# Optimization experiments

Measured on AMD Instinct MI355X. Metric: run time of the kernel, lower is better.

Reference implementation:

```python
import jax, jax.numpy as jnp
import numpy as np

# Constructor constants (init_kwargs)
DX = 10.0        # grid spacing [m]
DT = 0.001       # time step [s]
PML_FREQ = 15.0  # dominant frequency (used only for PML design in deepwave; see notes)
PML = 35         # pml_width
HALF = 4         # half-width of 8th-order stencil
NY, NX = 100, 200
NT = 300
N_SHOTS, N_SRC, N_REC = 2, 1, 100

# 8th-order central second-derivative coefficients, offsets -4..4
C2 = np.array([-1/560, 8/315, -1/5, 8/5, -205/72, 8/5, -1/5, 8/315, -1/560], np.float32)
# 8th-order central first-derivative coefficients, offsets -4..4
C1 = np.array([1/280, -4/105, 1/5, -4/5, 0.0, 4/5, -1/5, 4/105, -1/280], np.float32)


def shift_sum(u, coefs, axis):
    """Apply a 9-tap 1D stencil along `axis` (zero boundary outside the padded grid)."""
    pad = [(0, 0)] * u.ndim
    pad[axis] = (HALF, HALF)
    up = jnp.pad(u, pad)
    n = u.shape[axis]
    acc = jnp.zeros_like(u)
    for k in range(2 * HALF + 1):
        sl = [slice(None)] * u.ndim
        sl[axis] = slice(k, k + n)
        acc = acc + coefs[k] * up[tuple(sl)]
    return acc


def _sigma(n, vmax):
    # Quadratic PML damping profile, sigma_max from R=1e-3 reflection coefficient.
    d = jnp.arange(n, dtype=jnp.float32)
    r = jnp.maximum(jnp.maximum((PML - d) / PML, (d - (n - 1 - PML)) / PML), 0.0)
    smax = 3.0 * vmax * np.float32(np.log(1000.0)) / (2.0 * PML * DX)
    return smax * r * r


def _propagate(vp, src, src_loc, rec_loc):
    S, _, nt = src.shape
    v = jnp.pad(vp, PML, mode="edge")          # [ny, nx] padded grid
    ny, nx = v.shape
    v2 = (v * v)[None]                           # [1, ny, nx]
    vmax = jnp.max(vp)
    sy = _sigma(ny, vmax)
    sx = _sigma(nx, vmax)
    s = (sy[:, None] + sx[None, :])[None]        # combined damping
    pr = (sy[:, None] * sx[None, :])[None]       # corner cross term
    by = jnp.exp(-sy * DT)[None, :, None]        # CPML recursion factors
    bx = jnp.exp(-sx * DT)[None, None, :]
    c2 = jnp.asarray(C2) / np.float32(DX * DX)
    c1 = jnp.asarray(C1) / np.float32(DX)
    sids = jnp.arange(S)[:, None]
    syi = src_loc[..., 0] + PML
    sxi = src_loc[..., 1] + PML
    ryi = rec_loc[..., 0] + PML
    rxi = rec_loc[..., 1] + PML
    dt2 = np.float32(DT * DT)

    def step(carry, f_t):
        u, um, py, px = carry
        # CPML memory variables for the first derivatives
        py = by * py + (by - 1.0) * shift_sum(u, c1, 1)
        px = bx * px + (bx - 1.0) * shift_sum(u, c1, 2)
        lap = (shift_sum(u, c2, 1) + shift_sum(u, c2, 2)
               + shift_sum(py, c1, 1) + shift_sum(px, c1, 2))
        f = jnp.zeros_like(u).at[sids, syi, sxi].add(f_t)
        un = ((2.0 - pr * dt2) * u - (1.0 - 0.5 * s * DT) * um
              + dt2 * v2 * (lap + f)) / (1.0 + 0.5 * s * DT)
        rec = un[sids, ryi, rxi]                 # [S, n_rec]
        return (un, u, py, px), rec

    z = jnp.zeros((S, ny, nx), vp.dtype)
    xs = jnp.moveaxis(src, -1, 0)                # [nt, S, n_src]
    _, recs = jax.lax.scan(jax.checkpoint(step), (z, z, z, z), xs)
    return jnp.moveaxis(recs, 0, -1)             # [S, n_rec, nt]


def setup_inputs() -> dict:
    key = jax.random.key(0)
    k1, k2, k3, k4 = jax.random.split(key, 4)
    vp = 1500.0 + 2500.0 * jax.random.uniform(k1, (NY, NX), jnp.float32)
    src = jax.random.normal(k2, (N_SHOTS, N_SRC, NT), jnp.float32)
    src_loc = jax.random.randint(k3, (N_SHOTS, N_SRC, 2), 0, 90)
    rec_loc = jax.random.randint(k4, (N_SHOTS, N_REC, 2), 0, 90)
    return {"vp": vp, "src": src, "src_loc": src_loc, "rec_loc": rec_loc}


def reference(vp, src, src_loc, rec_loc):
    vx = _propagate(vp, src, src_loc, rec_loc)   # [S, n_rec, nt]
    # wrapper: vx.permute(0, 2, 1).unsqueeze(0) -> [1, S, nt, n_rec]
    return jnp.transpose(vx, (0, 2, 1))[None]
```

## Files before the change

### kernel.cpp

```cpp
#include <hip/hip_runtime.h>

constexpr int NY = 100, NX = 200;
constexpr int PML = 35;
constexpr int NYP = 170, NXP = 270;
constexpr int S = 2, NREC = 100, NT = 300;
constexpr float DX = 10.0f, DT = 1e-3f, DT2 = DT * DT;

constexpr int NTY = 16, NTX = 8;
constexpr int TY = 11, TX = 34;
constexpr int NBLKS = S * NTY * NTX;
constexpr int THREADS = 768;

constexpr int UTS = 35;
constexpr int UTSZ = TX * UTS;
constexpr int URS = 51;
constexpr int URSZ = TY * URS;
constexpr int PTS = 19;
constexpr int PTSZ = TX * PTS;
constexpr int PXS = 43;
constexpr int PXSZ = TY * PXS;
constexpr int BYW = TY + 8;
constexpr int BXW = TX + 8;

constexpr int CELLS_NS = 8 * TX;
constexpr int CELLS_WE = TY * 8;
constexpr int OFF_N = 0;
constexpr int OFF_S = CELLS_NS;
constexpr int OFF_W = 2 * CELLS_NS;
constexpr int OFF_E = 2 * CELLS_NS + CELLS_WE;
constexpr int STAGE_CELLS = 2 * CELLS_NS + 2 * CELLS_WE;

typedef unsigned long long u64;

__device__ __constant__ float C2D[9] = {
    (float)(-1.0/560.0/100.0), (float)(8.0/315.0/100.0), (float)(-1.0/5.0/100.0),
    (float)(8.0/5.0/100.0),    (float)(-205.0/72.0/100.0), (float)(8.0/5.0/100.0),
    (float)(-1.0/5.0/100.0),   (float)(8.0/315.0/100.0),  (float)(-1.0/560.0/100.0)};
__device__ __constant__ float C1D[9] = {
    (float)(1.0/280.0/10.0), (float)(-4.0/105.0/10.0), (float)(1.0/5.0/10.0),
    (float)(-4.0/5.0/10.0),  0.0f,                     (float)(4.0/5.0/10.0),
    (float)(-1.0/5.0/10.0),  (float)(4.0/105.0/10.0),  (float)(-1.0/280.0/10.0)};

__device__ __forceinline__ u64 gload64(const u64* p) {
    return __hip_atomic_load(p, __ATOMIC_RELAXED, __HIP_MEMORY_SCOPE_AGENT);
}
__device__ __forceinline__ void gstore64(u64* p, u64 v) {
    __hip_atomic_store(p, v, __ATOMIC_RELAXED, __HIP_MEMORY_SCOPE_AGENT);
}

__device__ __forceinline__ float sigma_of(int d, int n, float smax) {
    float r = fmaxf(fmaxf((float)(PML - d) / (float)PML,
                          (float)(d - (n - 1 - PML)) / (float)PML), 0.0f);
    return smax * r * r;
}

__global__ void vmax_kernel(const float* __restrict__ vp, float* __restrict__ cst) {
    __shared__ float red[256];
    float m = 0.0f;
    for (int i = threadIdx.x; i < NY * NX; i += 256) m = fmaxf(m, vp[i]);
    red[threadIdx.x] = m;
    __syncthreads();
    for (int s2 = 128; s2 > 0; s2 >>= 1) {
        if (threadIdx.x < s2) red[threadIdx.x] = fmaxf(red[threadIdx.x], red[threadIdx.x + s2]);
        __syncthreads();
    }
    if (threadIdx.x == 0)
        cst[0] = 3.0f * red[0] * logf(1000.0f) / (2.0f * PML * DX);
}

__global__ __launch_bounds__(THREADS) void persist_kernel(
    const float* __restrict__ vp, const float* __restrict__ src,
    const int* __restrict__ src_loc, const int* __restrict__ rec_loc,
    float* __restrict__ out, u64* __restrict__ stage,
    const float* __restrict__ cst) {

    __shared__ float uT[2][UTSZ];
    __shared__ float uR[2][URSZ];
    __shared__ float pyT[2][PTSZ];
    __shared__ float pxR[2][PXSZ];
    __shared__ float byS[BYW], bymS[BYW], bxS[BXW], bxmS[BXW];
    __shared__ float srcS[NT];

    const int tid = threadIdx.x;
    const int bid = blockIdx.x;
    const int sh  = bid / (NTY * NTX);
    const int tr  = bid - sh * (NTY * NTX);
    const int tyi = tr / NTX, txi = tr - tyi * NTX;
    const int y0 = tyi * TY, x0 = txi * TX;
    const int rows = min(TY, NYP - y0), cols = min(TX, NXP - x0);
    const float smax = cst[0];

    for (int i = tid; i < 2 * UTSZ; i += THREADS) ((float*)uT)[i] = 0.0f;
    for (int i = tid; i < 2 * URSZ; i += THREADS) ((float*)uR)[i] = 0.0f;
    for (int i = tid; i < 2 * PTSZ; i += THREADS) ((float*)pyT)[i] = 0.0f;
    for (int i = tid; i < 2 * PXSZ; i += THREADS) ((float*)pxR)[i] = 0.0f;

    if (tid < BYW) {
        int yy = y0 - 4 + tid;
        if (yy >= 0 && yy < NYP) {
            float b = __expf(-sigma_of(yy, NYP, smax) * DT);
            byS[tid] = b; bymS[tid] = b - 1.0f;
        } else { byS[tid] = 0.0f; bymS[tid] = 0.0f; }
    }
    if (tid < BXW) {
        int xx = x0 - 4 + tid;
        if (xx >= 0 && xx < NXP) {
            float b = __expf(-sigma_of(xx, NXP, smax) * DT);
            bxS[tid] = b; bxmS[tid] = b - 1.0f;
        } else { bxS[tid] = 0.0f; bxmS[tid] = 0.0f; }
    }

    const int role = tid & 1;
    const int cell = tid >> 1;
    const bool hasTask = (tid < 2 * rows * cols);
    const int y = hasTask ? cell / cols : 0;
    const int x = hasTask ? cell - y * cols : 0;

    float e_r = 0.0f, d_r = 0.0f, Av_r = 0.0f, Bv_r = 0.0f;
    if (hasTask) {
        int gy = y0 + y, gx = x0 + x;
        int vy = min(max(gy - PML, 0), NY - 1), vx = min(max(gx - PML, 0), NX - 1);
        float v = vp[vy * NX + vx];
        e_r = DT2 * v * v;
        float syv = sigma_of(gy, NYP, smax), sxv = sigma_of(gx, NXP, smax);
        d_r  = 1.0f / (1.0f + 0.5f * (syv + sxv) * DT);
        Av_r = 2.0f - syv * sxv * DT2;
        Bv_r = 1.0f - 0.5f * (syv + sxv) * DT;
    }

    const int sy = src_loc[sh * 2 + 0] + PML, sx = src_loc[sh * 2 + 1] + PML;
    const bool ownSrc = (sy >= y0 && sy < y0 + rows && sx >= x0 && sx < x0 + cols);
    const bool isSrc = hasTask && ownSrc && (y == sy - y0) && (x == sx - x0);
    if (ownSrc)
        for (int i = tid; i < NT; i += THREADS) srcS[i] = src[sh * NT + i];

    int recLds = -1, recOut = 0;
    if (tid < S * NREC) {
        int rs = tid / NREC, rr2 = tid - rs * NREC;
        int ry = rec_loc[(rs * NREC + rr2) * 2 + 0] + PML;
        int rx = rec_loc[(rs * NREC + rr2) * 2 + 1] + PML;
        if (rs == sh && ry >= y0 && ry < y0 + rows && rx >= x0 && rx < x0 + cols) {
            recLds = (ry - y0) * URS + (rx - x0 + 8);
            recOut = rs * NT * NREC + rr2;
        }
    }

    const int bN = (tyi > 0)       ? bid - NTX : -1;
    const int bS = (tyi < NTY - 1) ? bid + NTX : -1;
    const int bW = (txi > 0)       ? bid - 1   : -1;
    const int bE = (txi < NTX - 1) ? bid + 1   : -1;

    const int nNS = 8 * cols, nWE = rows * 8;
    const int nTot = 2 * nNS + 2 * nWE;

    int hOff = -1, hSrc = 0, hTgt = 0;
    if (tid < nTot) {
        int j = tid, nb = -1, o = 0, off = -1, tgt = 0;
        if (j < nNS) {
            nb = bN;
            int r2 = j / cols, c2 = j - r2 * cols;
            o = OFF_S + r2 * TX + c2;
            off = c2 * UTS + r2; tgt = 0;
        } else if ((j -= nNS) < nNS) {
            nb = bS;
            int r2 = j / cols, c2 = j - r2 * cols;
            if (nb >= 0) {
                int rowsS = min(TY, NYP - (y0 + TY));
                if (r2 >= rowsS) nb = -1;
            }
            o = OFF_N + r2 * TX + c2;
            off = c2 * UTS + (8 + rows + r2); tgt = 0;
        } else if ((j -= nNS) < nWE) {
            nb = bW;
            o = OFF_E + j;
            off = (j >> 3) * URS + (j & 7); tgt = 1;
        } else {
            j -= nWE;
            nb = bE;
            o = OFF_W + j;
            off = (j >> 3) * URS + 8 + cols + (j & 7); tgt = 1;
        }
        if (nb >= 0) { hOff = off; hTgt = tgt; hSrc = nb * 2 * STAGE_CELLS + o; }
    }
    const bool nv = (hOff >= 0);
    const u64* sA = stage + hSrc;

    int aN = -1, aS = -1, aW = -1, aE = -1;
    if (hasTask && role == 0) {
        if (y < 8)          aN = OFF_N + y * TX + x;
        if (y >= rows - 8)  aS = OFF_S + (y - (rows - 8)) * TX + x;
        if (x < 8)          aW = OFF_W + y * 8 + x;
        if (x >= cols - 8)  aE = OFF_E + y * 8 + (x - (cols - 8));
    }

    {
        const u64 PK0 = ((u64)1 << 32);
        u64* s0 = stage + (size_t)(bid * 2 + 0) * STAGE_CELLS;
        if (aN >= 0) gstore64(s0 + aN, PK0);
        if (aS >= 0) gstore64(s0 + aS, PK0);
        if (aW >= 0) gstore64(s0 + aW, PK0);
        if (aE >= 0) gstore64(s0 + aE, PK0);
    }
    __syncthreads();

    float wU[17], cbp[9];
    float bb0 = 0, bbm0 = 0, bb4 = 0, bbm4 = 0, bb8 = 0, bbm8 = 0;
    {
        float tb[9], tbm[9];
#pragma unroll
        for (int j = 0; j < 9; j++) {
            tb[j]  = hasTask ? (role ? bxS[x + j]  : byS[y + j])  : 0.0f;
            tbm[j] = hasTask ? (role ? bxmS[x + j] : bymS[y + j]) : 0.0f;
        }
#pragma unroll
        for (int n = 0; n < 17; n++) {
            float w = (n >= 4 && n <= 12) ? C2D[n - 4] : 0.0f;
#pragma unroll
            for (int k = 0; k < 9; k++) {
                int m = n - k;
                if (m >= 0 && m < 9)
                    w = fmaf(C1D[k] * tbm[k], C1D[m], w);
            }
            wU[n] = w;
        }
#pragma unroll
        for (int k = 0; k < 9; k++) cbp[k] = C1D[k] * tb[k];
        bb0 = tb[0]; bbm0 = tbm[0];
        bb4 = tb[4]; bbm4 = tbm[4];
        bb8 = tb[8]; bbm8 = tbm[8];
    }

    u64 pf = nv ? gload64(sA) : 0;

    float u_curr = 0.0f, u_prev = 0.0f;

    int pa = 0;
    for (int t = 0; t < NT; t++) {
        const int par = t & 1;
        float* uTc = uT[pa];       float* uRc = uR[pa];
        float* uTn = uT[pa ^ 1];   float* uRn = uR[pa ^ 1];
        const float* pyO = pyT[pa]; float* pyN = pyT[pa ^ 1];
        const float* pxO = pxR[pa]; float* pxN = pxR[pa ^ 1];

        if (nv) {
            const int need = t + 1;
            const u64* sp = sA + (size_t)par * STAGE_CELLS;
            while ((int)(pf >> 32) < need) pf = gload64(sp);
            (hTgt ? uRc : uTc)[hOff] = __uint_as_float((unsigned)pf);
        }
        __syncthreads();

        u64* sb = stage + (size_t)(bid * 2 + (par ^ 1)) * STAGE_CELLS;
        float up[17], pO[9], u_new = 0.0f;
        if (hasTask) {
            const float* uSrc = role ? &uRc[y * URS + x] : &uTc[x * UTS + y];
            const float* pSrc = role ? &pxO[y * PXS + x] : &pyO[x * PTS + y];

#pragma unroll
            for (int j = 0; j < 17; j++)
                up[j] = (j == 8) ? u_curr : uSrc[j];
#pragma unroll
            for (int k = 0; k < 9; k++) pO[k] = pSrc[k];

            float a0 = 0.0f, a1 = 0.0f, a2 = 0.0f, a3 = 0.0f;
#pragma unroll
            for (int n = 0; n < 16; n += 4) {
                a0 = fmaf(wU[n],     up[n],     a0);
                a1 = fmaf(wU[n + 1], up[n + 1], a1);
                a2 = fmaf(wU[n + 2], up[n + 2], a2);
                a3 = fmaf(wU[n + 3], up[n + 3], a3);
            }
            a0 = fmaf(wU[16], up[16], a0);
#pragma unroll
            for (int k = 0; k < 8; k += 4) {
                a0 = fmaf(cbp[k],     pO[k],     a0);
                a1 = fmaf(cbp[k + 1], pO[k + 1], a1);
                a2 = fmaf(cbp[k + 2], pO[k + 2], a2);
                a3 = fmaf(cbp[k + 3], pO[k + 3], a3);
            }
            a1 = fmaf(cbp[8], pO[8], a1);
            const float partial = (a0 + a1) + (a2 + a3);
            const float other = __shfl_xor(partial, 1);

            const float lap = partial + other;
            const float f = isSrc ? srcS[t] : 0.0f;
            u_new = (Av_r * u_curr - Bv_r * u_prev + e_r * (lap + f)) * d_r;

            const u64 pk = ((u64)(unsigned)(t + 2) << 32) |
                           (u64)__float_as_uint(u_new);
            if (aN >= 0) gstore64(sb + aN, pk);
            if (aS >= 0) gstore64(sb + aS, pk);
            if (aW >= 0) gstore64(sb + aW, pk);
            if (aE >= 0) gstore64(sb + aE, pk);
        }

        if (nv) pf = gload64(sA + (size_t)(par ^ 1) * STAGE_CELLS);

        if (hasTask) {
            float* pDst = role ? &pxR[pa ^ 1][y * PXS + x] : &pyT[pa ^ 1][x * PTS + y];
            float* uDst = role ? &uRn[y * URS + x + 8] : &uTn[x * UTS + y + 8];
            uDst[0] = u_new;
            {
                float d1u4 = 0.0f;
#pragma unroll
                for (int m = 0; m < 9; m++) d1u4 = fmaf(C1D[m], up[4 + m], d1u4);
                pDst[4] = fmaf(bb4, pO[4], bbm4 * d1u4);
            }
            const int lo = role ? x : y;
            const int hiLim = role ? cols : rows;
            if (lo < 4) {
                float d1u0 = 0.0f;
#pragma unroll
                for (int m = 0; m < 9; m++) d1u0 = fmaf(C1D[m], up[m], d1u0);
                pDst[0] = fmaf(bb0, pO[0], bbm0 * d1u0);
            }
            if (lo >= hiLim - 4) {
                float d1u8 = 0.0f;
#pragma unroll
                for (int m = 0; m < 9; m++) d1u8 = fmaf(C1D[m], up[8 + m], d1u8);
                pDst[8] = fmaf(bb8, pO[8], bbm8 * d1u8);
            }
            u_prev = u_curr; u_curr = u_new;
        }

        if (t > 0 && recLds >= 0) out[recOut + (t - 1) * NREC] = uRc[recLds];

        pa ^= 1;
    }

    __syncthreads();
    if (recLds >= 0) out[recOut + (NT - 1) * NREC] = uR[pa][recLds];
}

extern "C" void kernel_launch(void* const* d_in, const int* in_sizes, int n_in,
                              void* d_out, int out_size, void* d_ws, size_t ws_size,
                              hipStream_t stream) {
    const float* vp = (const float*)d_in[0];
    const float* src = (const float*)d_in[1];
    const int* src_loc = (const int*)d_in[2];
    const int* rec_loc = (const int*)d_in[3];
    float* out = (float*)d_out;

    float* ws = (float*)d_ws;
    float* cst = ws;
    u64* stage = (u64*)(ws + 32);

    hipMemsetAsync(d_ws, 0,
                   (size_t)32 * sizeof(float) +
                   (size_t)NBLKS * 2 * STAGE_CELLS * sizeof(u64),
                   stream);
    vmax_kernel<<<1, 256, 0, stream>>>(vp, cst);
    persist_kernel<<<NBLKS, THREADS, 0, stream>>>(
        vp, src, src_loc, rec_loc, out, stage, cst);
}
```

Before: 637.9 us.

## Register-block two cells per lane in 2x2 quads with shuffle-combined Laplacian

Each thread now computes a 1D stencil pass for two adjacent cells, so four lanes cover a 2x2 quad and exchange partial sums via shuffles. Loaded u and p windows are reused across both outputs, which cuts LDS reads per cell. The tile changes to 12x34 with 15 row blocks and 512 threads, and halo staging is spread over two entries per thread. It raises register pressure and makes every lane write both transposed u copies, and the quad mapping assumes even tile dimensions.

```diff
diff --git a/kernel.cpp b/kernel.cpp
--- a/kernel.cpp
+++ b/kernel.cpp
@@ -6,16 +6,16 @@
 constexpr int S = 2, NREC = 100, NT = 300;
 constexpr float DX = 10.0f, DT = 1e-3f, DT2 = DT * DT;
 
-constexpr int NTY = 16, NTX = 8;
-constexpr int TY = 11, TX = 34;
+constexpr int NTY = 15, NTX = 8;
+constexpr int TY = 12, TX = 34;
 constexpr int NBLKS = S * NTY * NTX;
-constexpr int THREADS = 768;
-
-constexpr int UTS = 35;
+constexpr int THREADS = 512;
+
+constexpr int UTS = 29;
 constexpr int UTSZ = TX * UTS;
 constexpr int URS = 51;
 constexpr int URSZ = TY * URS;
-constexpr int PTS = 19;
+constexpr int PTS = 21;
 constexpr int PTSZ = TX * PTS;
 constexpr int PXS = 43;
 constexpr int PXSZ = TY * PXS;
@@ -29,6 +29,7 @@
 constexpr int OFF_W = 2 * CELLS_NS;
 constexpr int OFF_E = 2 * CELLS_NS + CELLS_WE;
 constexpr int STAGE_CELLS = 2 * CELLS_NS + 2 * CELLS_WE;
+constexpr int NE = 2;
 
 typedef unsigned long long u64;
 
@@ -110,15 +111,20 @@
         } else { bxS[tid] = 0.0f; bxmS[tid] = 0.0f; }
     }
 
-    const int role = tid & 1;
-    const int cell = tid >> 1;
-    const bool hasTask = (tid < 2 * rows * cols);
-    const int y = hasTask ? cell / cols : 0;
-    const int x = hasTask ? cell - y * cols : 0;
+    const int l   = tid & 3;
+    const int qid = tid >> 2;
+    const int nQX = cols >> 1;
+    const int nQuads = (rows >> 1) * nQX;
+    const bool hasQ = (qid < nQuads);
+    const int qy = hasQ ? qid / nQX : 0;
+    const int qx = hasQ ? qid - qy * nQX : 0;
+    const bool isCol = (l < 2);
+    const int yp = 2 * qy + ((l == 1 || l == 3) ? 1 : 0);
+    const int xp = 2 * qx + ((l == 1 || l == 2) ? 1 : 0);
 
     float e_r = 0.0f, d_r = 0.0f, Av_r = 0.0f, Bv_r = 0.0f;
-    if (hasTask) {
-        int gy = y0 + y, gx = x0 + x;
+    if (hasQ) {
+        int gy = y0 + yp, gx = x0 + xp;
         int vy = min(max(gy - PML, 0), NY - 1), vx = min(max(gx - PML, 0), NX - 1);
         float v = vp[vy * NX + vx];
         e_r = DT2 * v * v;
@@ -130,7 +136,7 @@
 
     const int sy = src_loc[sh * 2 + 0] + PML, sx = src_loc[sh * 2 + 1] + PML;
     const bool ownSrc = (sy >= y0 && sy < y0 + rows && sx >= x0 && sx < x0 + cols);
-    const bool isSrc = hasTask && ownSrc && (y == sy - y0) && (x == sx - x0);
+    const bool isSrc = hasQ && ownSrc && (yp == sy - y0) && (xp == sx - x0);
     if (ownSrc)
         for (int i = tid; i < NT; i += THREADS) srcS[i] = src[sh * NT + i];
 
@@ -153,9 +159,14 @@
     const int nNS = 8 * cols, nWE = rows * 8;
     const int nTot = 2 * nNS + 2 * nWE;
 
-    int hOff = -1, hSrc = 0, hTgt = 0;
-    if (tid < nTot) {
-        int j = tid, nb = -1, o = 0, off = -1, tgt = 0;
+    int hOff[NE], hSrcI[NE], hTgt[NE];
+#pragma unroll
+    for (int e = 0; e < NE; e++) { hOff[e] = -1; hSrcI[e] = 0; hTgt[e] = 0; }
+#pragma unroll
+    for (int e = 0; e < NE; e++) {
+        int i = tid + e * THREADS;
+        if (i >= nTot) continue;
+        int j = i, nb = -1, o = 0, off = -1, tgt = 0;
         if (j < nNS) {
             nb = bN;
             int r2 = j / cols, c2 = j - r2 * cols;
@@ -180,17 +191,19 @@
             o = OFF_W + j;
             off = (j >> 3) * URS + 8 + cols + (j & 7); tgt = 1;
         }
-        if (nb >= 0) { hOff = off; hTgt = tgt; hSrc = nb * 2 * STAGE_CELLS + o; }
-    }
-    const bool nv = (hOff >= 0);
-    const u64* sA = stage + hSrc;
+        if (nb >= 0) { hOff[e] = off; hTgt[e] = tgt; hSrcI[e] = nb * 2 * STAGE_CELLS + o; }
+    }
+    bool nv[NE];
+    const u64* sA[NE];
+#pragma unroll
+    for (int e = 0; e < NE; e++) { nv[e] = (hOff[e] >= 0); sA[e] = stage + hSrcI[e]; }
 
     int aN = -1, aS = -1, aW = -1, aE = -1;
-    if (hasTask && role == 0) {
-        if (y < 8)          aN = OFF_N + y * TX + x;
-        if (y >= rows - 8)  aS = OFF_S + (y - (rows - 8)) * TX + x;
-        if (x < 8)          aW = OFF_W + y * 8 + x;
-        if (x >= cols - 8)  aE = OFF_E + y * 8 + (x - (cols - 8));
+    if (hasQ) {
+        if (yp < 8)          aN = OFF_N + yp * TX + xp;
+        if (yp >= rows - 8)  aS = OFF_S + (yp - (rows - 8)) * TX + xp;
+        if (xp < 8)          aW = OFF_W + yp * 8 + xp;
+        if (xp >= cols - 8)  aE = OFF_E + yp * 8 + (xp - (cols - 8));
     }
 
     {
@@ -203,34 +216,38 @@
     }
     __syncthreads();
 
-    float wU[17], cbp[9];
-    float bb0 = 0, bbm0 = 0, bb4 = 0, bbm4 = 0, bb8 = 0, bbm8 = 0;
-    {
-        float tb[9], tbm[9];
-#pragma unroll
-        for (int j = 0; j < 9; j++) {
-            tb[j]  = hasTask ? (role ? bxS[x + j]  : byS[y + j])  : 0.0f;
-            tbm[j] = hasTask ? (role ? bxmS[x + j] : bymS[y + j]) : 0.0f;
-        }
-#pragma unroll
-        for (int n = 0; n < 17; n++) {
-            float w = (n >= 4 && n <= 12) ? C2D[n - 4] : 0.0f;
-#pragma unroll
-            for (int k = 0; k < 9; k++) {
-                int m = n - k;
-                if (m >= 0 && m < 9)
-                    w = fmaf(C1D[k] * tbm[k], C1D[m], w);
-            }
-            wU[n] = w;
-        }
-#pragma unroll
-        for (int k = 0; k < 9; k++) cbp[k] = C1D[k] * tb[k];
-        bb0 = tb[0]; bbm0 = tbm[0];
-        bb4 = tb[4]; bbm4 = tbm[4];
-        bb8 = tb[8]; bbm8 = tbm[8];
-    }
-
-    u64 pf = nv ? gload64(sA) : 0;
+    const int base = isCol ? 2 * qy : 2 * qx;
+    const int lim  = isCol ? rows : cols;
+    float tb[10], tbm[10];
+#pragma unroll
+    for (int j = 0; j < 10; j++) {
+        tb[j]  = hasQ ? (isCol ? byS[base + j]  : bxS[base + j])  : 0.0f;
+        tbm[j] = hasQ ? (isCol ? bymS[base + j] : bxmS[base + j]) : 0.0f;
+    }
+    float wU0[17], wU1[17], cbp0[9], cbp1[9];
+#pragma unroll
+    for (int n = 0; n < 17; n++) {
+        float w0 = (n >= 4 && n <= 12) ? C2D[n - 4] : 0.0f;
+        float w1 = w0;
+#pragma unroll
+        for (int k = 0; k < 9; k++) {
+            int m = n - k;
+            if (m >= 0 && m < 9) {
+                w0 = fmaf(C1D[k] * tbm[k],     C1D[m], w0);
+                w1 = fmaf(C1D[k] * tbm[k + 1], C1D[m], w1);
+            }
+        }
+        wU0[n] = w0; wU1[n] = w1;
+    }
+#pragma unroll
+    for (int k = 0; k < 9; k++) {
+        cbp0[k] = C1D[k] * tb[k];
+        cbp1[k] = C1D[k] * tb[k + 1];
+    }
+
+    u64 pf[NE];
+#pragma unroll
+    for (int e = 0; e < NE; e++) pf[e] = nv[e] ? gload64(sA[e]) : 0;
 
     float u_curr = 0.0f, u_prev = 0.0f;
 
@@ -242,50 +259,79 @@
         const float* pyO = pyT[pa]; float* pyN = pyT[pa ^ 1];
         const float* pxO = pxR[pa]; float* pxN = pxR[pa ^ 1];
 
-        if (nv) {
+        {
             const int need = t + 1;
-            const u64* sp = sA + (size_t)par * STAGE_CELLS;
-            while ((int)(pf >> 32) < need) pf = gload64(sp);
-            (hTgt ? uRc : uTc)[hOff] = __uint_as_float((unsigned)pf);
+            for (;;) {
+                bool ok = true;
+#pragma unroll
+                for (int e = 0; e < NE; e++)
+                    if (nv[e] && (int)(pf[e] >> 32) < need) {
+                        pf[e] = gload64(sA[e] + (size_t)par * STAGE_CELLS);
+                        ok = false;
+                    }
+                if (ok) break;
+            }
+#pragma unroll
+            for (int e = 0; e < NE; e++)
+                if (nv[e]) (hTgt[e] ? uRc : uTc)[hOff[e]] = __uint_as_float((unsigned)pf[e]);
         }
         __syncthreads();
 
+        float uw[18], pw[10];
+        float p0 = 0.0f, p1 = 0.0f;
+        if (hasQ) {
+            const float* uW = isCol ? &uTc[(2 * qx + (l & 1)) * UTS + 2 * qy]
+                                    : &uRc[(2 * qy + (l & 1)) * URS + 2 * qx];
+            const float* pW = isCol ? &pyO[(2 * qx + (l & 1)) * PTS + 2 * qy]
+                                    : &pxO[(2 * qy + (l & 1)) * PXS + 2 * qx];
+#pragma unroll
+            for (int j = 0; j < 18; j++) uw[j] = uW[j];
+#pragma unroll
+            for (int k = 0; k < 10; k++) pw[k] = pW[k];
+
+            float a0 = 0, a1 = 0, a2 = 0, a3 = 0, b0 = 0, b1 = 0, b2 = 0, b3 = 0;
+#pragma unroll
+            for (int n = 0; n < 16; n += 4) {
+                a0 = fmaf(wU0[n],     uw[n],     a0);
+                a1 = fmaf(wU0[n + 1], uw[n + 1], a1);
+                a2 = fmaf(wU0[n + 2], uw[n + 2], a2);
+                a3 = fmaf(wU0[n + 3], uw[n + 3], a3);
+                b0 = fmaf(wU1[n],     uw[n + 1], b0);
+                b1 = fmaf(wU1[n + 1], uw[n + 2], b1);
+                b2 = fmaf(wU1[n + 2], uw[n + 3], b2);
+                b3 = fmaf(wU1[n + 3], uw[n + 4], b3);
+            }
+            a0 = fmaf(wU0[16], uw[16], a0);
+            b0 = fmaf(wU1[16], uw[17], b0);
+#pragma unroll
+            for (int k = 0; k < 8; k += 4) {
+                a0 = fmaf(cbp0[k],     pw[k],     a0);
+                a1 = fmaf(cbp0[k + 1], pw[k + 1], a1);
+                a2 = fmaf(cbp0[k + 2], pw[k + 2], a2);
+                a3 = fmaf(cbp0[k + 3], pw[k + 3], a3);
+                b0 = fmaf(cbp1[k],     pw[k + 1], b0);
+                b1 = fmaf(cbp1[k + 1], pw[k + 2], b1);
+                b2 = fmaf(cbp1[k + 2], pw[k + 3], b2);
+                b3 = fmaf(cbp1[k + 3], pw[k + 4], b3);
+            }
+            a1 = fmaf(cbp0[8], pw[8], a1);
+            b1 = fmaf(cbp1[8], pw[9], b1);
+            p0 = (a0 + a1) + (a2 + a3);
+            p1 = (b0 + b1) + (b2 + b3);
+        }
+
+        const float sh1 = __shfl_xor(p0, 2);
+        const float sh2 = __shfl_xor(p1, 2);
+        const float sh3 = __shfl_xor((l & 1) ? p0 : p1, 3);
+
         u64* sb = stage + (size_t)(bid * 2 + (par ^ 1)) * STAGE_CELLS;
-        float up[17], pO[9], u_new = 0.0f;
-        if (hasTask) {
-            const float* uSrc = role ? &uRc[y * URS + x] : &uTc[x * UTS + y];
-            const float* pSrc = role ? &pxO[y * PXS + x] : &pyO[x * PTS + y];
-
-#pragma unroll
-            for (int j = 0; j < 17; j++)
-                up[j] = (j == 8) ? u_curr : uSrc[j];
-#pragma unroll
-            for (int k = 0; k < 9; k++) pO[k] = pSrc[k];
-
-            float a0 = 0.0f, a1 = 0.0f, a2 = 0.0f, a3 = 0.0f;
-#pragma unroll
-            for (int n = 0; n < 16; n += 4) {
-                a0 = fmaf(wU[n],     up[n],     a0);
-                a1 = fmaf(wU[n + 1], up[n + 1], a1);
-                a2 = fmaf(wU[n + 2], up[n + 2], a2);
-                a3 = fmaf(wU[n + 3], up[n + 3], a3);
-            }
-            a0 = fmaf(wU[16], up[16], a0);
-#pragma unroll
-            for (int k = 0; k < 8; k += 4) {
-                a0 = fmaf(cbp[k],     pO[k],     a0);
-                a1 = fmaf(cbp[k + 1], pO[k + 1], a1);
-                a2 = fmaf(cbp[k + 2], pO[k + 2], a2);
-                a3 = fmaf(cbp[k + 3], pO[k + 3], a3);
-            }
-            a1 = fmaf(cbp[8], pO[8], a1);
-            const float partial = (a0 + a1) + (a2 + a3);
-            const float other = __shfl_xor(partial, 1);
-
-            const float lap = partial + other;
+        float u_new = 0.0f;
+        if (hasQ) {
+            const float lap = (l == 0) ? p0 + sh1 :
+                              (l == 1) ? p1 + sh2 :
+                              (l == 2) ? p1 + sh3 : p0 + sh3;
             const float f = isSrc ? srcS[t] : 0.0f;
             u_new = (Av_r * u_curr - Bv_r * u_prev + e_r * (lap + f)) * d_r;
-
             const u64 pk = ((u64)(unsigned)(t + 2) << 32) |
                            (u64)__float_as_uint(u_new);
             if (aN >= 0) gstore64(sb + aN, pk);
@@ -294,31 +340,43 @@
             if (aE >= 0) gstore64(sb + aE, pk);
         }
 
-        if (nv) pf = gload64(sA + (size_t)(par ^ 1) * STAGE_CELLS);
-
-        if (hasTask) {
-            float* pDst = role ? &pxR[pa ^ 1][y * PXS + x] : &pyT[pa ^ 1][x * PTS + y];
-            float* uDst = role ? &uRn[y * URS + x + 8] : &uTn[x * UTS + y + 8];
-            uDst[0] = u_new;
-            {
-                float d1u4 = 0.0f;
-#pragma unroll
-                for (int m = 0; m < 9; m++) d1u4 = fmaf(C1D[m], up[4 + m], d1u4);
-                pDst[4] = fmaf(bb4, pO[4], bbm4 * d1u4);
-            }
-            const int lo = role ? x : y;
-            const int hiLim = role ? cols : rows;
-            if (lo < 4) {
-                float d1u0 = 0.0f;
-#pragma unroll
-                for (int m = 0; m < 9; m++) d1u0 = fmaf(C1D[m], up[m], d1u0);
-                pDst[0] = fmaf(bb0, pO[0], bbm0 * d1u0);
-            }
-            if (lo >= hiLim - 4) {
-                float d1u8 = 0.0f;
-#pragma unroll
-                for (int m = 0; m < 9; m++) d1u8 = fmaf(C1D[m], up[8 + m], d1u8);
-                pDst[8] = fmaf(bb8, pO[8], bbm8 * d1u8);
+#pragma unroll
+        for (int e = 0; e < NE; e++)
+            if (nv[e]) pf[e] = gload64(sA[e] + (size_t)(par ^ 1) * STAGE_CELLS);
+
+        if (hasQ) {
+            uTn[xp * UTS + yp + 8] = u_new;
+            uRn[yp * URS + xp + 8] = u_new;
+
+            float* pD = isCol ? &pyN[(2 * qx + (l & 1)) * PTS + 2 * qy]
+                              : &pxN[(2 * qy + (l & 1)) * PXS + 2 * qx];
+            float dA = 0.0f, dB = 0.0f;
+#pragma unroll
+            for (int m = 0; m < 9; m++) {
+                dA = fmaf(C1D[m], uw[4 + m], dA);
+                dB = fmaf(C1D[m], uw[5 + m], dB);
+            }
+            pD[4] = fmaf(tb[4], pw[4], tbm[4] * dA);
+            pD[5] = fmaf(tb[5], pw[5], tbm[5] * dB);
+            if (base < 4) {
+                float d0 = 0.0f, d1 = 0.0f;
+#pragma unroll
+                for (int m = 0; m < 9; m++) {
+                    d0 = fmaf(C1D[m], uw[m], d0);
+                    d1 = fmaf(C1D[m], uw[1 + m], d1);
+                }
+                pD[0] = fmaf(tb[0], pw[0], tbm[0] * d0);
+                pD[1] = fmaf(tb[1], pw[1], tbm[1] * d1);
+            }
+            if (base >= lim - 4) {
+                float d8 = 0.0f, d9 = 0.0f;
+#pragma unroll
+                for (int m = 0; m < 9; m++) {
+                    d8 = fmaf(C1D[m], uw[8 + m], d8);
+                    d9 = fmaf(C1D[m], uw[9 + m], d9);
+                }
+                pD[8] = fmaf(tb[8], pw[8], tbm[8] * d8);
+                pD[9] = fmaf(tb[9], pw[9], tbm[9] * d9);
             }
             u_prev = u_curr; u_curr = u_new;
         }
```

Result: slower. 838.4 us (+31.4%).
